# Performance work log

Hardware: AMD Instinct MI355X
Metric: run time of the kernel (lower is better)

## Reference

```python
import jax, jax.numpy as jnp
import numpy as np

B, N, IN, OUT, H = 16, 1024, 512, 512, 4

def setup_inputs() -> dict:
    key = jax.random.key(0)
    ks = jax.random.split(key, 10)
    s = 0.03  # small init scale to keep tanh/sigmoid in sane range
    return {
        "h": jax.random.normal(ks[0], (B, N, IN), jnp.float32),
        "adj": jax.random.randint(ks[1], (B, N, N), 0, 2) > 0,
        "W": jax.random.normal(ks[2], (H, OUT, IN), jnp.float32) * s,   # per-head Linear weight [out,in]
        "bW": jax.random.normal(ks[3], (H, OUT), jnp.float32) * s,
        "attn": jax.random.normal(ks[4], (H, OUT, OUT), jnp.float32) * s,
        "A_w": jax.random.normal(ks[5], (OUT, OUT * H), jnp.float32) * s,
        "fc_w": jax.random.normal(ks[6], (OUT, IN), jnp.float32) * s,
        "g1_w": jax.random.normal(ks[7], (OUT, OUT), jnp.float32) * s,
        "g2_w": jax.random.normal(ks[8], (OUT, OUT), jnp.float32) * s,
        "gbias": jax.random.normal(ks[9], (OUT,), jnp.float32) * s,
    }

def reference(h, adj, W, bW, attn, A_w, fc_w, g1_w, g2_w, gbias):
    # Per-head projection: Wh[b,h,n,o] = h @ W_h^T + b_h  (dropout is identity at inference)
    Wh = jnp.einsum('bni,hoi->bhno', h, W) + bW[None, :, None, :]
    # Bilinear attention scores: Wh @ attn_h @ Wh^T, masked by adjacency, then tanh
    e = jnp.einsum('bhno,hop->bhnp', Wh, attn)          # [B,H,N,O]
    scores = jnp.einsum('bhnp,bhmp->bhnm', e, Wh)       # [B,H,N,N]
    A_mat = jnp.tanh(jnp.where(adj[:, None, :, :], scores, 0.0))
    # Aggregate neighbors and relu
    hp = jax.nn.relu(jnp.einsum('bhnm,bhmo->bhno', A_mat, Wh))  # [B,H,N,O]
    # Concat heads (relu of relu is identity), project with A
    cat = jnp.transpose(hp, (0, 2, 1, 3)).reshape(hp.shape[0], hp.shape[2], -1)  # [B,N,H*O]
    ha = cat @ A_w.T                                     # [B,N,O]
    hf = h @ fc_w.T                                      # [B,N,O]
    # Sigmoid-gated fusion of the two branches
    coeff = jax.nn.sigmoid(hf @ g1_w.T + ha @ g2_w.T + gbias)
    return hf * coeff + ha * (1.0 - coeff)
```

## Files before the change

kernel.cpp:

```cpp
#include <hip/hip_runtime.h>
#include <hip/hip_fp16.h>


typedef _Float16 h8 __attribute__((ext_vector_type(8)));
typedef _Float16 h4 __attribute__((ext_vector_type(4)));
typedef float f4 __attribute__((ext_vector_type(4)));

__device__ __forceinline__ void load_lds16(const void* g, void* l) {
  __builtin_amdgcn_global_load_lds(
      (const __attribute__((address_space(1))) unsigned int*)g,
      (__attribute__((address_space(3))) unsigned int*)l, 16, 0, 0);
}

struct GP {
  const _Float16* A; const _Float16* B; void* C; const float* bias;
  const unsigned long long* adjb; _Float16* aux;
  int K, ldA, ldB, ldC, z0, ntx, nty, nz;
  long sAz, sAb, sBz, sBh, sCz, sCb, sCh, sBiasH, sAuxZ;
};

__device__ __forceinline__ void stage_tiles5(const _Float16* Ag, const _Float16* Bg,
                                             _Float16* As, _Float16* Bs,
                                             int ldA, int ldB, int wv, int rs, int cs) {
#pragma unroll
  for (int ps = 0; ps < 10; ++ps) {
    int c = ps * 4 + wv;
    if (c < 8) {
      int r = c * 8 + rs;
      int kb = (cs ^ (r & 7)) * 8;
      load_lds16(Ag + (long)r * ldA + kb, As + c * 512);
    } else {
      int cb = c - 8;
      int r = cb * 8 + rs;
      int kb = (cs ^ (r & 7)) * 8;
      load_lds16(Bg + (long)r * ldB + kb, Bs + cb * 512);
    }
  }
}

__device__ __forceinline__ void compute_tile5(const _Float16* As, const _Float16* Bs,
                                              f4 acc[4][4], int wv, int l15, int lg) {
#pragma unroll
  for (int ks = 0; ks < 2; ++ks) {
    const int kby = ks * 64 + lg * 16;
    h8 av[4], bv[4];
#pragma unroll
    for (int m = 0; m < 4; ++m) {
      int row = m * 16 + l15;
      av[m] = *(const h8*)((const char*)As + row * 128 + (kby ^ ((row & 7) << 4)));
    }
#pragma unroll
    for (int n = 0; n < 4; ++n) {
      int col = wv * 64 + n * 16 + l15;
      bv[n] = *(const h8*)((const char*)Bs + col * 128 + (kby ^ ((col & 7) << 4)));
    }
#pragma unroll
    for (int m = 0; m < 4; ++m)
#pragma unroll
      for (int n = 0; n < 4; ++n)
        acc[m][n] = __builtin_amdgcn_mfma_f32_16x16x32_f16(av[m], bv[n], acc[m][n], 0, 0, 0);
  }
}

template<int EPI>
__device__ __forceinline__ void gemm_core(GP p) {
  __shared__ __align__(16) char smem[40960];
  _Float16* Ash = (_Float16*)smem;
  _Float16* Bsh = (_Float16*)(smem + 8192);
  _Float16* Cld = (_Float16*)smem;

  const int tid = threadIdx.x;
  const int wv = tid >> 6;
  const int ln = tid & 63;
  const int l15 = ln & 15;
  const int lg = ln >> 4;
  const int rs = ln >> 3;
  const int cs = ln & 7;

  const int bid = blockIdx.x;
  const int ntile = p.ntx * p.nty;
  int zl, tx, ty;
  if (p.nz > 1) {
    int xcd = bid & 7;
    int u = bid >> 3;
    zl = xcd + 8 * (u / ntile);
    int t = u % ntile;
    tx = t % p.ntx;
    ty = t / p.ntx;
  } else {
    int xcd = bid & 7;
    int u = bid >> 3;
    int t = xcd * (ntile >> 3) + u;
    zl = 0;
    tx = t % p.ntx;
    ty = t / p.ntx;
  }
  const int zg = p.z0 + zl;
  const int bg = zg >> 2, hg = zg & 3;
  const _Float16* A = p.A + p.sAz * zl + p.sAb * bg;
  const _Float16* Bm = p.B + p.sBz * zl + p.sBh * hg;
  const long m0 = (long)tx * 64;
  const long n0 = (long)ty * 256;
  const int nk = p.K >> 6;

  f4 acc[4][4];
#pragma unroll
  for (int i = 0; i < 4; ++i)
#pragma unroll
    for (int j = 0; j < 4; ++j) acc[i][j] = (f4)(0.0f);

  const _Float16* Ag = A + m0 * p.ldA;
  const _Float16* Bg = Bm + n0 * p.ldB;

  for (int kt = 0; kt < nk; ++kt) {
    stage_tiles5(Ag + kt * 64, Bg + kt * 64, Ash, Bsh, p.ldA, p.ldB, wv, rs, cs);
    __syncthreads();
    compute_tile5(Ash, Bsh, acc, wv, l15, lg);
    __syncthreads();
  }

  const long coff = p.sCz * zl + p.sCb * bg + p.sCh * hg;
  const float* bias = p.bias ? (p.bias + p.sBiasH * hg) : nullptr;
  _Float16* C = (_Float16*)p.C;
  _Float16* X = (EPI == 6) ? (p.aux + p.sAuxZ * zl) : nullptr;
#pragma unroll
  for (int m = 0; m < 4; ++m) {
#pragma unroll
    for (int j = 0; j < 4; ++j) {
      int lrow = m * 16 + lg * 4 + j;
      long grow = m0 + lrow;
      int vx = (lrow & 3) << 4;
      unsigned long long w;
      if (EPI == 2)
        w = p.adjb[(long)bg * 16384 + grow * 16 + (n0 >> 6) + wv];
#pragma unroll
      for (int n = 0; n < 4; ++n) {
        int lcol = wv * 64 + n * 16 + l15;
        float v = acc[m][n][j];
        if (EPI == 5 || EPI == 6) v += bias[n0 + lcol];
        if (EPI == 2) {
          if ((w >> (n * 16 + l15)) & 1ull) {
            float ex = __expf(2.0f * v);
            v = 1.0f - 2.0f * __builtin_amdgcn_rcpf(ex + 1.0f);
          } else v = 0.0f;
        }
        if (EPI == 3) v = v > 0.0f ? v : 0.0f;
        if (EPI == 5) v = __builtin_amdgcn_rcpf(1.0f + __expf(-v));
        Cld[lrow * 256 + (lcol ^ vx)] = (_Float16)v;
      }
    }
  }
  __syncthreads();
#pragma unroll
  for (int it = 0; it < 8; ++it) {
    int row = it * 8 + (tid >> 5);
    int col0 = (tid & 31) * 8;
    int vx = (row & 3) << 4;
    h8 o = *(const h8*)&Cld[row * 256 + (col0 ^ vx)];
    *(h8*)&C[coff + (m0 + row) * p.ldC + n0 + col0] = o;
  }
  if (EPI == 6) {
#pragma unroll
    for (int it = 0; it < 8; ++it) {
      int idx = it * 256 + tid;
      int ol = idx >> 3;
      int ml = (idx & 7) * 8;
      h8 o;
#pragma unroll
      for (int j = 0; j < 8; ++j) {
        int mm = ml + j;
        o[j] = Cld[mm * 256 + (ol ^ ((mm & 3) << 4))];
      }
      *(h8*)&X[(n0 + ol) * 1024 + m0 + ml] = o;
    }
  }
}

#define GEMM_WRAP(name, epi) \
  __global__ __launch_bounds__(256) void name(GP p) { gemm_core<epi>(p); }
GEMM_WRAP(gemm_wh, 6)
GEMM_WRAP(gemm_e, 0)
GEMM_WRAP(gemm_amat, 2)
GEMM_WRAP(gemm_cat, 3)
GEMM_WRAP(gemm_hf, 0)
GEMM_WRAP(gemm_ha, 0)
GEMM_WRAP(gemm_gate, 5)

__global__ __launch_bounds__(256) void mix_kernel(const _Float16* gcat,
                                                  const _Float16* coeff, float* out) {
  const int stride = gridDim.x * 256;
  for (int g = blockIdx.x * 256 + threadIdx.x; g < 1048576; g += stride) {
    int r = g >> 6, c8 = (g & 63) << 3;
    h8 hf = *(const h8*)&gcat[(long)r * 1024 + c8];
    h8 ha = *(const h8*)&gcat[(long)r * 1024 + 512 + c8];
    h8 cf = *(const h8*)&coeff[(long)r * 512 + c8];
    float o[8];
#pragma unroll
    for (int j = 0; j < 8; ++j) {
      float c = (float)cf[j];
      o[j] = (float)hf[j] * c + (float)ha[j] * (1.0f - c);
    }
    float* op = &out[(long)r * 512 + c8];
    *(float4*)op = make_float4(o[0], o[1], o[2], o[3]);
    *(float4*)(op + 4) = make_float4(o[4], o[5], o[6], o[7]);
  }
}

__global__ void trans_attn(const float* attn, _Float16* attnT) {
  __shared__ _Float16 tl[64][65];
  const long hh = blockIdx.z;
  const float* I = attn + hh * 262144;
  _Float16* O = attnT + hh * 262144;
  const int r0 = blockIdx.x * 64, c0 = blockIdx.y * 64;
  for (int i = threadIdx.x; i < 4096; i += 256) {
    int r = i >> 6, c = i & 63;
    tl[c][r] = (_Float16)I[(long)(r0 + r) * 512 + c0 + c];
  }
  __syncthreads();
  for (int i = threadIdx.x; i < 4096; i += 256) {
    int c = i >> 6, r = i & 63;
    O[(long)(c0 + c) * 512 + r0 + r] = tl[c][r];
  }
}

__global__ void cvt_f16(const float* in, _Float16* out, int n4) {
  int i = blockIdx.x * 256 + threadIdx.x;
  if (i < n4) {
    float4 v = ((const float4*)in)[i];
    h4 o = {(_Float16)v.x, (_Float16)v.y, (_Float16)v.z, (_Float16)v.w};
    ((h4*)out)[i] = o;
  }
}

__global__ void build_gw(const float* g1, const float* g2, _Float16* gw) {
  int i = blockIdx.x * 256 + threadIdx.x;
  int o = i >> 10, k = i & 1023;
  float v = (k < 512) ? g1[o * 512 + k] : g2[o * 512 + (k - 512)];
  gw[i] = (_Float16)v;
}

__global__ void detect_fmt(const unsigned char* adj, int* flags) {
  __shared__ int sa, sb, sc;
  if (threadIdx.x == 0) { sa = 0; sb = 0; sc = 0; }
  __syncthreads();
  int a = 0, b = 0, c = 0;
  for (int i = threadIdx.x; i < 4096; i += 256) {
    if (adj[i]) {
      if (i & 3) a = 1;
      else c = 1;
      if ((i & 7) == 4) b = 1;
    }
  }
  if (a) sa = 1;
  if (b) sb = 1;
  if (c) sc = 1;
  __syncthreads();
  if (threadIdx.x == 0) {
    int fmt;
    if (sa) fmt = sc ? 1 : 3;
    else fmt = sb ? 0 : 2;
    flags[0] = fmt;
  }
}

__global__ void adj_bits(const void* adj, const int* flags, unsigned long long* adjb) {
  long i = (long)blockIdx.x * 256 + threadIdx.x;
  int fmt = flags[0];
  bool v;
  if (fmt == 1) v = ((const unsigned char*)adj)[i] != 0;
  else if (fmt == 3) v = ((const float*)adj)[i] != 0.0f;
  else if (fmt == 2) v = ((const long long*)adj)[i] != 0;
  else v = ((const int*)adj)[i] != 0;
  unsigned long long m = __ballot(v);
  if ((threadIdx.x & 63) == 0) adjb[i >> 6] = m;
}

extern "C" void kernel_launch(void* const* d_in, const int* in_sizes, int n_in,
                              void* d_out, int out_size, void* d_ws, size_t ws_size,
                              hipStream_t stream) {
  const float* h    = (const float*)d_in[0];
  const void*  adj  = d_in[1];
  const float* W    = (const float*)d_in[2];
  const float* bW   = (const float*)d_in[3];
  const float* attn = (const float*)d_in[4];
  const float* A_w  = (const float*)d_in[5];
  const float* fc_w = (const float*)d_in[6];
  const float* g1   = (const float*)d_in[7];
  const float* g2   = (const float*)d_in[8];
  const float* gbias= (const float*)d_in[9];
  float* out = (float*)d_out;
  char* ws = (char*)d_ws;
  (void)in_sizes; (void)n_in; (void)out_size;

  const size_t MB = 1ull << 20;
  const size_t fixedB = 92 * MB;
  int ZCv = 16;
  if (fixedB + 5ull * 64 * MB <= ws_size) ZCv = 64;
  else if (fixedB + 5ull * 32 * MB <= ws_size) ZCv = 32;
  const int nchunk = 64 / ZCv;

  size_t off = 0;
  auto alloc = [&](size_t sz) { size_t o = off; off += (sz + 255) & ~(size_t)255; return o; };
  const size_t oFlags = alloc(256);
  const size_t oH16   = alloc(16 * MB);
  const size_t oW16   = alloc(2 * MB);
  const size_t oAttnT = alloc(2 * MB);
  const size_t oAw16  = alloc(2 * MB);
  const size_t oFc16  = alloc(512 * 1024);
  const size_t oGw16  = alloc(1 * MB);
  const size_t oAdjb  = alloc(2 * MB);
  const size_t oCat   = alloc(64 * MB);
  const size_t oWhC   = alloc((size_t)ZCv * MB);
  const size_t oEC    = alloc((size_t)ZCv * MB);
  const size_t oWhTC  = alloc((size_t)ZCv * MB);
  const size_t oAmatC = alloc((size_t)ZCv * 2 * MB);
  const size_t oGcat  = oWhC;
  const size_t oCoeff = oAmatC;

  int* flags = (int*)(ws + oFlags);
  _Float16* h16   = (_Float16*)(ws + oH16);
  _Float16* W16   = (_Float16*)(ws + oW16);
  _Float16* attnT = (_Float16*)(ws + oAttnT);
  _Float16* Aw16  = (_Float16*)(ws + oAw16);
  _Float16* fc16  = (_Float16*)(ws + oFc16);
  _Float16* gw16  = (_Float16*)(ws + oGw16);
  unsigned long long* adjb = (unsigned long long*)(ws + oAdjb);
  _Float16* cat   = (_Float16*)(ws + oCat);
  _Float16* WhC   = (_Float16*)(ws + oWhC);
  _Float16* eC    = (_Float16*)(ws + oEC);
  _Float16* WhTC  = (_Float16*)(ws + oWhTC);
  _Float16* AmatC = (_Float16*)(ws + oAmatC);
  _Float16* gcat  = (_Float16*)(ws + oGcat);
  _Float16* coeff = (_Float16*)(ws + oCoeff);

  detect_fmt<<<1, 256, 0, stream>>>((const unsigned char*)adj, flags);
  adj_bits<<<65536, 256, 0, stream>>>(adj, flags, adjb);
  cvt_f16<<<8192, 256, 0, stream>>>(h, h16, 2097152);
  cvt_f16<<<1024, 256, 0, stream>>>(W, W16, 262144);
  cvt_f16<<<1024, 256, 0, stream>>>(A_w, Aw16, 262144);
  cvt_f16<<<256, 256, 0, stream>>>(fc_w, fc16, 65536);
  build_gw<<<2048, 256, 0, stream>>>(g1, g2, gw16);
  trans_attn<<<dim3(8, 8, 4), 256, 0, stream>>>(attn, attnT);

  for (int c = 0; c < nchunk; ++c) {
    const int z0 = c * ZCv;
    GP q;
    q = GP{};
    q.A = h16; q.B = W16; q.C = WhC; q.bias = bW; q.aux = WhTC;
    q.K = 512; q.ldA = 512; q.ldB = 512; q.ldC = 512; q.z0 = z0;
    q.ntx = 16; q.nty = 2; q.nz = ZCv;
    q.sAz = 0; q.sAb = 524288; q.sBz = 0; q.sBh = 262144;
    q.sCz = 524288; q.sCb = 0; q.sCh = 0; q.sBiasH = 512; q.sAuxZ = 524288;
    gemm_wh<<<32 * ZCv, 256, 0, stream>>>(q);
    q = GP{};
    q.A = WhC; q.B = attnT; q.C = eC;
    q.K = 512; q.ldA = 512; q.ldB = 512; q.ldC = 512; q.z0 = z0;
    q.ntx = 16; q.nty = 2; q.nz = ZCv;
    q.sAz = 524288; q.sBh = 262144; q.sCz = 524288;
    gemm_e<<<32 * ZCv, 256, 0, stream>>>(q);
    q = GP{};
    q.A = eC; q.B = WhC; q.C = AmatC; q.adjb = adjb;
    q.K = 512; q.ldA = 512; q.ldB = 512; q.ldC = 1024; q.z0 = z0;
    q.ntx = 16; q.nty = 4; q.nz = ZCv;
    q.sAz = 524288; q.sBz = 524288; q.sCz = 1048576;
    gemm_amat<<<64 * ZCv, 256, 0, stream>>>(q);
    q = GP{};
    q.A = AmatC; q.B = WhTC; q.C = cat;
    q.K = 1024; q.ldA = 1024; q.ldB = 1024; q.ldC = 2048; q.z0 = z0;
    q.sAz = 1048576; q.sBz = 524288;
    q.ntx = 16; q.nty = 2; q.nz = ZCv;
    q.sCz = 0; q.sCb = 2097152; q.sCh = 512;
    gemm_cat<<<32 * ZCv, 256, 0, stream>>>(q);
  }

  GP q;
  q = GP{};
  q.A = h16; q.B = fc16; q.C = gcat;
  q.K = 512; q.ldA = 512; q.ldB = 512; q.ldC = 1024; q.z0 = 0;
  q.ntx = 256; q.nty = 2; q.nz = 1;
  gemm_hf<<<512, 256, 0, stream>>>(q);
  q = GP{};
  q.A = cat; q.B = Aw16; q.C = gcat + 512;
  q.K = 2048; q.ldA = 2048; q.ldB = 2048; q.ldC = 1024; q.z0 = 0;
  q.ntx = 256; q.nty = 2; q.nz = 1;
  gemm_ha<<<512, 256, 0, stream>>>(q);
  q = GP{};
  q.A = gcat; q.B = gw16; q.C = coeff; q.bias = gbias;
  q.K = 1024; q.ldA = 1024; q.ldB = 1024; q.ldC = 512; q.z0 = 0;
  q.ntx = 256; q.nty = 2; q.nz = 1; q.sBiasH = 0;
  gemm_gate<<<512, 256, 0, stream>>>(q);
  mix_kernel<<<2048, 256, 0, stream>>>(gcat, coeff, out);
}
```

Before: 496.5 us.

## Add triple-buffered 128x256 pipelined GEMM with 512 threads for per-head stages

Replaces the single-buffered 64x256 GEMM used for the four per-head batched GEMMs with a 512-thread, 128x256-tile kernel. It triple-buffers LDS stages through async global-to-LDS loads, using explicit vmcnt waits, barriers interleaved with MFMA phases, and setprio. The goal is to overlap memory loads with MFMA work and raise reuse per tile, at the cost of 144KB of dynamic LDS per block (one block per CU) and half as many blocks. The final dense GEMMs keep a simplified single-buffer kernel.

```diff
diff --git a/kernel.cpp b/kernel.cpp
--- a/kernel.cpp
+++ b/kernel.cpp
@@ -19,61 +19,21 @@
   long sAz, sAb, sBz, sBh, sCz, sCb, sCh, sBiasH, sAuxZ;
 };
 
-__device__ __forceinline__ void stage_tiles5(const _Float16* Ag, const _Float16* Bg,
-                                             _Float16* As, _Float16* Bs,
-                                             int ldA, int ldB, int wv, int rs, int cs) {
-#pragma unroll
-  for (int ps = 0; ps < 10; ++ps) {
-    int c = ps * 4 + wv;
-    if (c < 8) {
-      int r = c * 8 + rs;
-      int kb = (cs ^ (r & 7)) * 8;
-      load_lds16(Ag + (long)r * ldA + kb, As + c * 512);
-    } else {
-      int cb = c - 8;
-      int r = cb * 8 + rs;
-      int kb = (cs ^ (r & 7)) * 8;
-      load_lds16(Bg + (long)r * ldB + kb, Bs + cb * 512);
-    }
-  }
-}
-
-__device__ __forceinline__ void compute_tile5(const _Float16* As, const _Float16* Bs,
-                                              f4 acc[4][4], int wv, int l15, int lg) {
-#pragma unroll
-  for (int ks = 0; ks < 2; ++ks) {
-    const int kby = ks * 64 + lg * 16;
-    h8 av[4], bv[4];
-#pragma unroll
-    for (int m = 0; m < 4; ++m) {
-      int row = m * 16 + l15;
-      av[m] = *(const h8*)((const char*)As + row * 128 + (kby ^ ((row & 7) << 4)));
-    }
-#pragma unroll
-    for (int n = 0; n < 4; ++n) {
-      int col = wv * 64 + n * 16 + l15;
-      bv[n] = *(const h8*)((const char*)Bs + col * 128 + (kby ^ ((col & 7) << 4)));
-    }
-#pragma unroll
-    for (int m = 0; m < 4; ++m)
-#pragma unroll
-      for (int n = 0; n < 4; ++n)
-        acc[m][n] = __builtin_amdgcn_mfma_f32_16x16x32_f16(av[m], bv[n], acc[m][n], 0, 0, 0);
-  }
+__device__ __forceinline__ void stage_chunk(const _Float16* G, long ld, int koff,
+                                            _Float16* S, int c, int rs, int cs) {
+  int r = c * 8 + rs;
+  int kb = (cs ^ (r & 7)) * 8;
+  load_lds16(G + (long)r * ld + koff + kb, S + c * 512);
 }
 
 template<int EPI>
-__device__ __forceinline__ void gemm_core(GP p) {
-  __shared__ __align__(16) char smem[40960];
-  _Float16* Ash = (_Float16*)smem;
-  _Float16* Bsh = (_Float16*)(smem + 8192);
-  _Float16* Cld = (_Float16*)smem;
-
+__device__ __forceinline__ void gemm_pipe(GP p, char* smem) {
   const int tid = threadIdx.x;
   const int wv = tid >> 6;
   const int ln = tid & 63;
   const int l15 = ln & 15;
   const int lg = ln >> 4;
+  const int wr = wv >> 2, wc = wv & 3;
   const int rs = ln >> 3;
   const int cs = ln & 7;
 
@@ -99,6 +59,240 @@
   const int bg = zg >> 2, hg = zg & 3;
   const _Float16* A = p.A + p.sAz * zl + p.sAb * bg;
   const _Float16* Bm = p.B + p.sBz * zl + p.sBh * hg;
+  const long m0 = (long)tx * 128;
+  const long n0 = (long)ty * 256;
+  const int nk = p.K >> 6;
+
+  const _Float16* Ag = A + m0 * p.ldA;
+  const _Float16* Bg = Bm + n0 * p.ldB;
+
+  f4 acc[4][4];
+#pragma unroll
+  for (int i = 0; i < 4; ++i)
+#pragma unroll
+    for (int j = 0; j < 4; ++j) acc[i][j] = (f4)(0.0f);
+
+#define ABUF(i) ((_Float16*)(smem + (i) * 49152))
+#define BBUF(i) ((_Float16*)(smem + (i) * 49152 + 16384))
+
+#pragma unroll
+  for (int t0 = 0; t0 < 2; ++t0) {
+    if (t0 < nk) {
+      _Float16* As = ABUF(t0);
+      _Float16* Bs = BBUF(t0);
+      const int ko = t0 * 64;
+      stage_chunk(Bg, p.ldB, ko, Bs, wv * 2, rs, cs);
+      stage_chunk(Bg, p.ldB, ko, Bs, wv * 2 + 1, rs, cs);
+      stage_chunk(Bg, p.ldB, ko, Bs, 16 + wv * 2, rs, cs);
+      stage_chunk(Bg, p.ldB, ko, Bs, 16 + wv * 2 + 1, rs, cs);
+      stage_chunk(Ag, p.ldA, ko, As, wv * 2, rs, cs);
+      stage_chunk(Ag, p.ldA, ko, As, wv * 2 + 1, rs, cs);
+    }
+  }
+  if (nk > 1) asm volatile("s_waitcnt vmcnt(6)" ::: "memory");
+  else        asm volatile("s_waitcnt vmcnt(0)" ::: "memory");
+  __builtin_amdgcn_sched_barrier(0);
+  __builtin_amdgcn_s_barrier();
+
+  for (int t = 0; t < nk; ++t) {
+    _Float16* As = ABUF(t % 3);
+    _Float16* Bs = BBUF(t % 3);
+    const int t2 = t + 2;
+    const bool st = (t2 < nk);
+    _Float16* As2 = ABUF(t2 % 3);
+    _Float16* Bs2 = BBUF(t2 % 3);
+    const int ko2 = t2 * 64;
+#pragma unroll
+    for (int ph = 0; ph < 4; ++ph) {
+      if (st) {
+        if (ph == 0) {
+          stage_chunk(Bg, p.ldB, ko2, Bs2, wv * 2, rs, cs);
+          stage_chunk(Bg, p.ldB, ko2, Bs2, wv * 2 + 1, rs, cs);
+        } else if (ph == 1) {
+          stage_chunk(Bg, p.ldB, ko2, Bs2, 16 + wv * 2, rs, cs);
+          stage_chunk(Bg, p.ldB, ko2, Bs2, 16 + wv * 2 + 1, rs, cs);
+        } else if (ph == 2) {
+          stage_chunk(Ag, p.ldA, ko2, As2, wv * 2, rs, cs);
+          stage_chunk(Ag, p.ldA, ko2, As2, wv * 2 + 1, rs, cs);
+        }
+      }
+      const int ks = ph >> 1, mp = ph & 1;
+      const int kby = ks * 64 + lg * 16;
+      h8 av[2], bv[4];
+#pragma unroll
+      for (int m2 = 0; m2 < 2; ++m2) {
+        int row = wr * 64 + (mp * 2 + m2) * 16 + l15;
+        av[m2] = *(const h8*)((const char*)As + row * 128 + (kby ^ ((row & 7) << 4)));
+      }
+#pragma unroll
+      for (int n = 0; n < 4; ++n) {
+        int col = wc * 64 + n * 16 + l15;
+        bv[n] = *(const h8*)((const char*)Bs + col * 128 + (kby ^ ((col & 7) << 4)));
+      }
+      __builtin_amdgcn_s_barrier();
+      __builtin_amdgcn_s_setprio(1);
+#pragma unroll
+      for (int m2 = 0; m2 < 2; ++m2)
+#pragma unroll
+        for (int n = 0; n < 4; ++n)
+          acc[mp * 2 + m2][n] =
+              __builtin_amdgcn_mfma_f32_16x16x32_f16(av[m2], bv[n], acc[mp * 2 + m2][n], 0, 0, 0);
+      __builtin_amdgcn_s_setprio(0);
+    }
+    if (t + 1 < nk) {
+      if (t + 2 < nk) asm volatile("s_waitcnt vmcnt(6)" ::: "memory");
+      else            asm volatile("s_waitcnt vmcnt(0)" ::: "memory");
+      __builtin_amdgcn_sched_barrier(0);
+      __builtin_amdgcn_s_barrier();
+    }
+  }
+
+  asm volatile("s_waitcnt vmcnt(0)" ::: "memory");
+  __syncthreads();
+
+  _Float16* Cld = (_Float16*)smem;
+  const long coff = p.sCz * zl + p.sCb * bg + p.sCh * hg;
+  const float* bias = p.bias ? (p.bias + p.sBiasH * hg) : nullptr;
+  _Float16* C = (_Float16*)p.C;
+  _Float16* X = (EPI == 6) ? (p.aux + p.sAuxZ * zl) : nullptr;
+#pragma unroll
+  for (int hh = 0; hh < 2; ++hh) {
+    if (wr == hh) {
+#pragma unroll
+      for (int m = 0; m < 4; ++m) {
+#pragma unroll
+        for (int j = 0; j < 4; ++j) {
+          int lrow = m * 16 + lg * 4 + j;
+          long grow = m0 + hh * 64 + lrow;
+          int vx = (lrow & 3) << 4;
+          unsigned long long w;
+          if (EPI == 2)
+            w = p.adjb[(long)bg * 16384 + grow * 16 + (n0 >> 6) + wc];
+#pragma unroll
+          for (int n = 0; n < 4; ++n) {
+            int lcol = wv * 0 + wc * 64 + n * 16 + l15;
+            float v = acc[m][n][j];
+            if (EPI == 6) v += bias[n0 + lcol];
+            if (EPI == 2) {
+              if ((w >> (n * 16 + l15)) & 1ull) {
+                float ex = __expf(2.0f * v);
+                v = 1.0f - 2.0f * __builtin_amdgcn_rcpf(ex + 1.0f);
+              } else v = 0.0f;
+            }
+            if (EPI == 3) v = v > 0.0f ? v : 0.0f;
+            Cld[lrow * 256 + (lcol ^ vx)] = (_Float16)v;
+          }
+        }
+      }
+    }
+    __syncthreads();
+#pragma unroll
+    for (int it = 0; it < 4; ++it) {
+      int row = it * 16 + (tid >> 5);
+      int col0 = (tid & 31) * 8;
+      int vx = (row & 3) << 4;
+      h8 o = *(const h8*)&Cld[row * 256 + (col0 ^ vx)];
+      *(h8*)&C[coff + (m0 + hh * 64 + row) * p.ldC + n0 + col0] = o;
+    }
+    if (EPI == 6) {
+#pragma unroll
+      for (int it = 0; it < 4; ++it) {
+        int idx = it * 512 + tid;
+        int ol = idx >> 3;
+        int ml = (idx & 7) * 8;
+        h8 o;
+#pragma unroll
+        for (int j = 0; j < 8; ++j) {
+          int mm = ml + j;
+          o[j] = Cld[mm * 256 + (ol ^ ((mm & 3) << 4))];
+        }
+        *(h8*)&X[(n0 + ol) * 1024 + m0 + hh * 64 + ml] = o;
+      }
+    }
+    __syncthreads();
+  }
+#undef ABUF
+#undef BBUF
+}
+
+#define GEMM_PIPE_WRAP(name, epi)                                      \
+  __global__ __launch_bounds__(512) void name(GP p) {                  \
+    extern __shared__ char smem[];                                     \
+    gemm_pipe<epi>(p, smem);                                           \
+  }
+GEMM_PIPE_WRAP(gemm_wh, 6)
+GEMM_PIPE_WRAP(gemm_e, 0)
+GEMM_PIPE_WRAP(gemm_amat, 2)
+GEMM_PIPE_WRAP(gemm_cat, 3)
+
+__device__ __forceinline__ void stage_tiles5(const _Float16* Ag, const _Float16* Bg,
+                                             _Float16* As, _Float16* Bs,
+                                             int ldA, int ldB, int wv, int rs, int cs) {
+#pragma unroll
+  for (int ps = 0; ps < 10; ++ps) {
+    int c = ps * 4 + wv;
+    if (c < 8) {
+      int r = c * 8 + rs;
+      int kb = (cs ^ (r & 7)) * 8;
+      load_lds16(Ag + (long)r * ldA + kb, As + c * 512);
+    } else {
+      int cb = c - 8;
+      int r = cb * 8 + rs;
+      int kb = (cs ^ (r & 7)) * 8;
+      load_lds16(Bg + (long)r * ldB + kb, Bs + cb * 512);
+    }
+  }
+}
+
+__device__ __forceinline__ void compute_tile5(const _Float16* As, const _Float16* Bs,
+                                              f4 acc[4][4], int wv, int l15, int lg) {
+#pragma unroll
+  for (int ks = 0; ks < 2; ++ks) {
+    const int kby = ks * 64 + lg * 16;
+    h8 av[4], bv[4];
+#pragma unroll
+    for (int m = 0; m < 4; ++m) {
+      int row = m * 16 + l15;
+      av[m] = *(const h8*)((const char*)As + row * 128 + (kby ^ ((row & 7) << 4)));
+    }
+#pragma unroll
+    for (int n = 0; n < 4; ++n) {
+      int col = wv * 64 + n * 16 + l15;
+      bv[n] = *(const h8*)((const char*)Bs + col * 128 + (kby ^ ((col & 7) << 4)));
+    }
+#pragma unroll
+    for (int m = 0; m < 4; ++m)
+#pragma unroll
+      for (int n = 0; n < 4; ++n)
+        acc[m][n] = __builtin_amdgcn_mfma_f32_16x16x32_f16(av[m], bv[n], acc[m][n], 0, 0, 0);
+  }
+}
+
+template<int EPI>
+__device__ __forceinline__ void gemm_core_sb(GP p) {
+  __shared__ __align__(16) char smem[40960];
+  _Float16* Ash = (_Float16*)smem;
+  _Float16* Bsh = (_Float16*)(smem + 8192);
+  _Float16* Cld = (_Float16*)smem;
+
+  const int tid = threadIdx.x;
+  const int wv = tid >> 6;
+  const int ln = tid & 63;
+  const int l15 = ln & 15;
+  const int lg = ln >> 4;
+  const int rs = ln >> 3;
+  const int cs = ln & 7;
+
+  const int bid = blockIdx.x;
+  const int ntile = p.ntx * p.nty;
+  int xcd = bid & 7;
+  int u = bid >> 3;
+  int t = xcd * (ntile >> 3) + u;
+  int tx = t % p.ntx;
+  int ty = t / p.ntx;
+  const int bg = 0, hg = 0;
+  const _Float16* A = p.A;
+  const _Float16* Bm = p.B;
   const long m0 = (long)tx * 64;
   const long n0 = (long)ty * 256;
   const int nk = p.K >> 6;
@@ -119,33 +313,23 @@
     __syncthreads();
   }
 
-  const long coff = p.sCz * zl + p.sCb * bg + p.sCh * hg;
-  const float* bias = p.bias ? (p.bias + p.sBiasH * hg) : nullptr;
+  const long coff = 0;
+  const float* bias = p.bias;
   _Float16* C = (_Float16*)p.C;
-  _Float16* X = (EPI == 6) ? (p.aux + p.sAuxZ * zl) : nullptr;
 #pragma unroll
   for (int m = 0; m < 4; ++m) {
 #pragma unroll
     for (int j = 0; j < 4; ++j) {
       int lrow = m * 16 + lg * 4 + j;
-      long grow = m0 + lrow;
       int vx = (lrow & 3) << 4;
-      unsigned long long w;
-      if (EPI == 2)
-        w = p.adjb[(long)bg * 16384 + grow * 16 + (n0 >> 6) + wv];
 #pragma unroll
       for (int n = 0; n < 4; ++n) {
         int lcol = wv * 64 + n * 16 + l15;
         float v = acc[m][n][j];
-        if (EPI == 5 || EPI == 6) v += bias[n0 + lcol];
-        if (EPI == 2) {
-          if ((w >> (n * 16 + l15)) & 1ull) {
-            float ex = __expf(2.0f * v);
-            v = 1.0f - 2.0f * __builtin_amdgcn_rcpf(ex + 1.0f);
-          } else v = 0.0f;
+        if (EPI == 5) {
+          v += bias[n0 + lcol];
+          v = __builtin_amdgcn_rcpf(1.0f + __expf(-v));
         }
-        if (EPI == 3) v = v > 0.0f ? v : 0.0f;
-        if (EPI == 5) v = __builtin_amdgcn_rcpf(1.0f + __expf(-v));
         Cld[lrow * 256 + (lcol ^ vx)] = (_Float16)v;
       }
     }
@@ -159,32 +343,14 @@
     h8 o = *(const h8*)&Cld[row * 256 + (col0 ^ vx)];
     *(h8*)&C[coff + (m0 + row) * p.ldC + n0 + col0] = o;
   }
-  if (EPI == 6) {
-#pragma unroll
-    for (int it = 0; it < 8; ++it) {
-      int idx = it * 256 + tid;
-      int ol = idx >> 3;
-      int ml = (idx & 7) * 8;
-      h8 o;
-#pragma unroll
-      for (int j = 0; j < 8; ++j) {
-        int mm = ml + j;
-        o[j] = Cld[mm * 256 + (ol ^ ((mm & 3) << 4))];
-      }
-      *(h8*)&X[(n0 + ol) * 1024 + m0 + ml] = o;
-    }
-  }
-}
-
-#define GEMM_WRAP(name, epi) \
-  __global__ __launch_bounds__(256) void name(GP p) { gemm_core<epi>(p); }
-GEMM_WRAP(gemm_wh, 6)
-GEMM_WRAP(gemm_e, 0)
-GEMM_WRAP(gemm_amat, 2)
-GEMM_WRAP(gemm_cat, 3)
-GEMM_WRAP(gemm_hf, 0)
-GEMM_WRAP(gemm_ha, 0)
-GEMM_WRAP(gemm_gate, 5)
+  (void)bg; (void)hg;
+}
+
+#define GEMM_SB_WRAP(name, epi) \
+  __global__ __launch_bounds__(256) void name(GP p) { gemm_core_sb<epi>(p); }
+GEMM_SB_WRAP(gemm_hf, 0)
+GEMM_SB_WRAP(gemm_ha, 0)
+GEMM_SB_WRAP(gemm_gate, 5)
 
 __global__ __launch_bounds__(256) void mix_kernel(const _Float16* gcat,
                                                   const _Float16* coeff, float* out) {
@@ -291,6 +457,12 @@
   float* out = (float*)d_out;
   char* ws = (char*)d_ws;
   (void)in_sizes; (void)n_in; (void)out_size;
+
+  const int PIPE_LDS = 147456;
+  hipFuncSetAttribute((const void*)gemm_wh,   hipFuncAttributeMaxDynamicSharedMemorySize, PIPE_LDS);
+  hipFuncSetAttribute((const void*)gemm_e,    hipFuncAttributeMaxDynamicSharedMemorySize, PIPE_LDS);
+  hipFuncSetAttribute((const void*)gemm_amat, hipFuncAttributeMaxDynamicSharedMemorySize, PIPE_LDS);
+  hipFuncSetAttribute((const void*)gemm_cat,  hipFuncAttributeMaxDynamicSharedMemorySize, PIPE_LDS);
 
   const size_t MB = 1ull << 20;
   const size_t fixedB = 92 * MB;
@@ -348,29 +520,29 @@
     q = GP{};
     q.A = h16; q.B = W16; q.C = WhC; q.bias = bW; q.aux = WhTC;
     q.K = 512; q.ldA = 512; q.ldB = 512; q.ldC = 512; q.z0 = z0;
-    q.ntx = 16; q.nty = 2; q.nz = ZCv;
+    q.ntx = 8; q.nty = 2; q.nz = ZCv;
     q.sAz = 0; q.sAb = 524288; q.sBz = 0; q.sBh = 262144;
     q.sCz = 524288; q.sCb = 0; q.sCh = 0; q.sBiasH = 512; q.sAuxZ = 524288;
-    gemm_wh<<<32 * ZCv, 256, 0, stream>>>(q);
+    gemm_wh<<<16 * ZCv, 512, PIPE_LDS, stream>>>(q);
     q = GP{};
     q.A = WhC; q.B = attnT; q.C = eC;
     q.K = 512; q.ldA = 512; q.ldB = 512; q.ldC = 512; q.z0 = z0;
-    q.ntx = 16; q.nty = 2; q.nz = ZCv;
+    q.ntx = 8; q.nty = 2; q.nz = ZCv;
     q.sAz = 524288; q.sBh = 262144; q.sCz = 524288;
-    gemm_e<<<32 * ZCv, 256, 0, stream>>>(q);
+    gemm_e<<<16 * ZCv, 512, PIPE_LDS, stream>>>(q);
     q = GP{};
     q.A = eC; q.B = WhC; q.C = AmatC; q.adjb = adjb;
     q.K = 512; q.ldA = 512; q.ldB = 512; q.ldC = 1024; q.z0 = z0;
-    q.ntx = 16; q.nty = 4; q.nz = ZCv;
+    q.ntx = 8; q.nty = 4; q.nz = ZCv;
     q.sAz = 524288; q.sBz = 524288; q.sCz = 1048576;
-    gemm_amat<<<64 * ZCv, 256, 0, stream>>>(q);
+    gemm_amat<<<32 * ZCv, 512, PIPE_LDS, stream>>>(q);
     q = GP{};
     q.A = AmatC; q.B = WhTC; q.C = cat;
     q.K = 1024; q.ldA = 1024; q.ldB = 1024; q.ldC = 2048; q.z0 = z0;
     q.sAz = 1048576; q.sBz = 524288;
-    q.ntx = 16; q.nty = 2; q.nz = ZCv;
+    q.ntx = 8; q.nty = 2; q.nz = ZCv;
     q.sCz = 0; q.sCb = 2097152; q.sCh = 512;
-    gemm_cat<<<32 * ZCv, 256, 0, stream>>>(q);
+    gemm_cat<<<16 * ZCv, 512, PIPE_LDS, stream>>>(q);
   }
 
   GP q;
@@ -387,7 +559,7 @@
   q = GP{};
   q.A = gcat; q.B = gw16; q.C = coeff; q.bias = gbias;
   q.K = 1024; q.ldA = 1024; q.ldB = 1024; q.ldC = 512; q.z0 = 0;
-  q.ntx = 256; q.nty = 2; q.nz = 1; q.sBiasH = 0;
+  q.ntx = 256; q.nty = 2; q.nz = 1;
   gemm_gate<<<512, 256, 0, stream>>>(q);
   mix_kernel<<<2048, 256, 0, stream>>>(gcat, coeff, out);
 }
```

After: 537.0 us. 8.2% more time.
